# Performance work log

Hardware: AMD Instinct MI355X
Metric: run time of the kernel (lower is better)

## Reference

```python
import jax, jax.numpy as jnp
from jax import lax
import numpy as np

N_BLOCKS = 5; C = 256; K = 1024; NQ = 8; NRES = 4; B = 2; T = 65536


def conv1d(x, w, b, stride=1, padding=0, dilation=1):
    # x: [N,C,T], w: [O,I,k]
    y = lax.conv_general_dilated(x, w, (stride,), [(padding, padding)],
                                 rhs_dilation=(dilation,),
                                 dimension_numbers=('NCH', 'OIH', 'NCH'))
    return y + b[None, :, None]


def conv_transpose1d(x, w, b):
    # PyTorch ConvTranspose1d(k=4, s=2, p=1); w: [in, out, 4]
    wk = jnp.swapaxes(jnp.flip(w, -1), 0, 1)  # [out, in, 4]
    y = lax.conv_general_dilated(x, wk, (1,), [(2, 2)], lhs_dilation=(2,),
                                 dimension_numbers=('NCH', 'OIH', 'NCH'))
    return y + b[None, :, None]


def residual_model(x, w0, b0, w1, b1, dil):
    # ReLU -> dilated conv3 -> ReLU -> conv3
    h = conv1d(jax.nn.relu(x), w0, b0, padding=dil, dilation=dil)
    h = conv1d(jax.nn.relu(h), w1, b1, padding=1)
    return h


def encoder(x, d0w, d0b, dw, db, rw, rb):
    for i in range(N_BLOCKS):
        if i == 0:
            x = conv1d(x, d0w, d0b, stride=2, padding=1)
        else:
            x = conv1d(x, dw[i - 1], db[i - 1], stride=2, padding=1)
        for j in range(NRES):
            dil = 3 ** (j + 1)
            # ResidualBlock.forward: x + model(x)
            x = x + residual_model(x, rw[i, j, 0], rb[i, j, 0], rw[i, j, 1], rb[i, j, 1], dil)
    return x


def decoder(x, rw, rb, uw, ub, ulw, ulb):
    for i in range(N_BLOCKS):
        for j in range(NRES):
            dil = 3 ** (j + 1)
            # DecoderBlock: x = x + ResidualBlock(x) = x + (x + model(x))
            x = x + (x + residual_model(x, rw[i, j, 0], rb[i, j, 0], rw[i, j, 1], rb[i, j, 1], dil))
        if i == N_BLOCKS - 1:
            x = conv_transpose1d(x, ulw, ulb)
        else:
            x = conv_transpose1d(x, uw[i], ub[i])
    return x


def rvq(emb, rvq_sum, rvq_usage):
    # emb: [N, C]; eval-mode residual VQ (no EMA update)
    q = jnp.zeros_like(emb)
    commit = jnp.asarray(0.0, emb.dtype)
    codes = []
    for i in range(NQ):
        cb = rvq_sum[i] / jnp.clip(rvq_usage[i], 1e-5, None)[:, None]  # [K, C]
        res = emb - q
        # argmin of squared distance over codebook rows (||res||^2 constant per column)
        scores = jnp.sum(cb * cb, axis=1)[:, None] - 2.0 * (cb @ res.T)  # [K, N]
        c = jnp.argmin(scores, axis=0)
        eq = cb[c]  # [N, C]
        eq_st = res + lax.stop_gradient(eq - res)  # straight-through
        commit = commit + jnp.mean((lax.stop_gradient(eq_st) - res) ** 2)
        q = q + eq_st
        codes.append(c.astype(jnp.int32))
    return jnp.stack(codes, axis=1), q, commit


def setup_inputs() -> dict:
    key = jax.random.key(0)
    ks = iter(jax.random.split(key, 16))

    def W(shape, fan_in):
        return (jax.random.normal(next(ks), shape, jnp.float32) / np.float32(np.sqrt(fan_in)))

    return {
        'x': jax.random.normal(next(ks), (B, 1, T), jnp.float32),
        'enc_down0_w': W((C, 1, 4), 4),
        'enc_down0_b': jnp.zeros((C,), jnp.float32),
        'enc_down_w': W((N_BLOCKS - 1, C, C, 4), C * 4),
        'enc_down_b': jnp.zeros((N_BLOCKS - 1, C), jnp.float32),
        'enc_res_w': W((N_BLOCKS, NRES, 2, C, C, 3), C * 3),
        'enc_res_b': jnp.zeros((N_BLOCKS, NRES, 2, C), jnp.float32),
        'dec_res_w': W((N_BLOCKS, NRES, 2, C, C, 3), C * 3),
        'dec_res_b': jnp.zeros((N_BLOCKS, NRES, 2, C), jnp.float32),
        'dec_up_w': W((N_BLOCKS - 1, C, C, 4), C * 4),
        'dec_up_b': jnp.zeros((N_BLOCKS - 1, C), jnp.float32),
        'dec_up_last_w': W((C, 1, 4), C * 4),
        'dec_up_last_b': jnp.zeros((1,), jnp.float32),
        'rvq_sum': jax.random.normal(next(ks), (NQ, K, C), jnp.float32) * 0.1,
        'rvq_usage': jnp.ones((NQ, K), jnp.float32),
    }


def reference(x, enc_down0_w, enc_down0_b, enc_down_w, enc_down_b, enc_res_w, enc_res_b,
              dec_res_w, dec_res_b, dec_up_w, dec_up_b, dec_up_last_w, dec_up_last_b,
              rvq_sum, rvq_usage):
    z = encoder(x, enc_down0_w, enc_down0_b, enc_down_w, enc_down_b, enc_res_w, enc_res_b)
    Bz, Cz, Tz = z.shape
    emb = jnp.transpose(z, (0, 2, 1)).reshape(Bz * Tz, Cz)  # (b t) c
    codes, q, commit = rvq(emb, rvq_sum, rvq_usage)
    zq = jnp.transpose(q.reshape(Bz, Tz, Cz), (0, 2, 1))  # b c t
    recon = decoder(zq, dec_res_w, dec_res_b, dec_up_w, dec_up_b, dec_up_last_w, dec_up_last_b)
    return recon, codes, commit
```

## Files before the change

### kernel.cpp

```cpp
#include <hip/hip_runtime.h>
#include <cstdint>

#define DEVFN static __device__ __forceinline__
typedef unsigned short ushort_t;
typedef unsigned int uint_t;
typedef short short8 __attribute__((ext_vector_type(8)));
typedef float f32x4 __attribute__((ext_vector_type(4)));

DEVFN float bf2f(ushort_t h) { return __uint_as_float(((uint_t)h) << 16); }
DEVFN ushort_t bfhi(float f) {
    uint_t u = __float_as_uint(f);
    u += 0x7fffu + ((u >> 16) & 1u);
    return (ushort_t)(u >> 16);
}
DEVFN void fsplit(float f, ushort_t& h, ushort_t& l) {
    h = bfhi(f);
    l = bfhi(f - bf2f(h));
}
DEVFN void relu_pair(uint_t& h, uint_t& l) {
    float f0 = bf2f((ushort_t)(h & 0xffffu)) + bf2f((ushort_t)(l & 0xffffu));
    float f1 = bf2f((ushort_t)(h >> 16)) + bf2f((ushort_t)(l >> 16));
    if (f0 <= 0.f) { h &= 0xffff0000u; l &= 0xffff0000u; }
    if (f1 <= 0.f) { h &= 0x0000ffffu; l &= 0x0000ffffu; }
}

__global__ __launch_bounds__(256)
void wprep3_k(const float* __restrict__ erw, const float* __restrict__ drw,
              ushort_t* __restrict__ wH, ushort_t* __restrict__ wL)
{
    const int gid = blockIdx.x * 256 + threadIdx.x;
    const int conv = gid >> 16;
    const int rem  = gid & 65535;
    const int co = rem >> 8, ci = rem & 255;
    const float* src = (conv < 40) ? (erw + (size_t)conv * 196608)
                                   : (drw + (size_t)(conv - 40) * 196608);
    const float* p = src + ((size_t)co * 256 + ci) * 3;
    ushort_t* oh = wH + (size_t)conv * 196608 + rem;
    ushort_t* ol = wL + (size_t)conv * 196608 + rem;
#pragma unroll
    for (int k = 0; k < 3; ++k) {
        ushort_t h, l; fsplit(p[k], h, l);
        oh[k * 65536] = h; ol[k * 65536] = l;
    }
}

__global__ __launch_bounds__(256)
void wprep4_k(const float* __restrict__ edw, const float* __restrict__ duw,
              ushort_t* __restrict__ wH, ushort_t* __restrict__ wL)
{
    const int gid = blockIdx.x * 256 + threadIdx.x;
    const int conv = gid >> 16;
    const int rem  = gid & 65535;
    const int co = rem >> 8, ci = rem & 255;
    ushort_t* oh = wH + (size_t)conv * 262144 + rem;
    ushort_t* ol = wL + (size_t)conv * 262144 + rem;
#pragma unroll
    for (int k = 0; k < 4; ++k) {
        float f;
        if (conv < 4)  f = edw[(size_t)conv * 262144 + ((size_t)co * 256 + ci) * 4 + k];
        else           f = duw[(size_t)(conv - 4) * 262144 + ((size_t)ci * 256 + co) * 4 + k];
        ushort_t h, l; fsplit(f, h, l);
        oh[k * 65536] = h; ol[k * 65536] = l;
    }
}

template<int TAPS, int STRIDE, bool RELU, int NT, int DMAX, bool DBUF>
__global__ __launch_bounds__(256, (NT >= 8) ? 2 : 3)
void convs_k(const ushort_t* __restrict__ inH, const ushort_t* __restrict__ inL,
             const ushort_t* __restrict__ wH, const ushort_t* __restrict__ wL,
             const float* __restrict__ bias,
             const ushort_t* __restrict__ srcH, const ushort_t* __restrict__ srcL,
             float alpha,
             ushort_t* __restrict__ outH, ushort_t* __restrict__ outL,
             int Lin, int Lout, int dil, int pad)
{
    constexpr int ROWS = NT * 16;
    constexpr int SMAX = STRIDE * (ROWS - 1) + (TAPS - 1) * DMAX + 1;
    constexpr int XSB  = SMAX * 80;
    constexpr int NEED = DBUF ? 4 * XSB : 2 * XSB;
    constexpr int ARENA = (NEED > 16640) ? NEED : 16640;
    static_assert(!DBUF || (4 * SMAX <= TAPS * 256), "prefetch item budget");
    __shared__ __align__(16) char sarena[ARENA];

    const int tid = threadIdx.x;
    const int b = blockIdx.z;
    const int t0 = blockIdx.x * ROWS;
    const int wave = tid >> 6, lane = tid & 63;
    const int quad = lane >> 4, lr = lane & 15;
    const int cow = wave * 64;
    const size_t inbase = (size_t)b * Lin * 256;
    const int S = STRIDE * (ROWS - 1) + (TAPS - 1) * dil + 1;
    const int g0 = STRIDE * t0 - pad;

    f32x4 acc[4][NT];
#pragma unroll
    for (int m = 0; m < 4; ++m)
#pragma unroll
        for (int n = 0; n < NT; ++n) acc[m][n] = (f32x4)0.f;

    if constexpr (DBUF) {
        ushort_t (*xsH0)[40] = (ushort_t(*)[40])(sarena);
        ushort_t (*xsL0)[40] = (ushort_t(*)[40])(sarena + XSB);
        ushort_t (*xsH1)[40] = (ushort_t(*)[40])(sarena + 2 * XSB);
        ushort_t (*xsL1)[40] = (ushort_t(*)[40])(sarena + 3 * XSB);
        for (int idx = tid; idx < S * 4; idx += 256) {
            const int s = idx >> 2, p = idx & 3;
            const int t = g0 + s;
            uint4 hv = make_uint4(0, 0, 0, 0), lv = hv;
            if (t >= 0 && t < Lin) {
                const size_t g = inbase + (size_t)t * 256 + p * 8;
                hv = *(const uint4*)(inH + g);
                lv = *(const uint4*)(inL + g);
                if (RELU) {
                    relu_pair(hv.x, lv.x); relu_pair(hv.y, lv.y);
                    relu_pair(hv.z, lv.z); relu_pair(hv.w, lv.w);
                }
            }
            *(uint4*)&xsH0[s][p * 8] = hv;
            *(uint4*)&xsL0[s][p * 8] = lv;
        }
        __syncthreads();
        for (int chunk = 0; chunk < 8; ++chunk) {
            const int ci0 = chunk * 32;
            ushort_t (*xsH)[40] = (chunk & 1) ? xsH1 : xsH0;
            ushort_t (*xsL)[40] = (chunk & 1) ? xsL1 : xsL0;
            ushort_t (*xnH)[40] = (chunk & 1) ? xsH0 : xsH1;
            ushort_t (*xnL)[40] = (chunk & 1) ? xsL0 : xsL1;
            const bool pf = (chunk < 7);
#pragma unroll
            for (int tap = 0; tap < TAPS; ++tap) {
                const ushort_t* wHt = wH + (size_t)tap * 65536 + ci0 + quad * 8;
                const ushort_t* wLt = wL + (size_t)tap * 65536 + ci0 + quad * 8;
                short8 aH[4], aL[4];
#pragma unroll
                for (int m = 0; m < 4; ++m) {
                    const int co = cow + m * 16 + lr;
                    aH[m] = *(const short8*)(wHt + co * 256);
                    aL[m] = *(const short8*)(wLt + co * 256);
                }
                const int idx = tap * 256 + tid;
                const int s = idx >> 2, p = idx & 3;
                const int tr = g0 + s;
                const bool inr = (idx < S * 4);
                uint4 hv = make_uint4(0, 0, 0, 0), lv = hv;
                if (pf && inr && tr >= 0 && tr < Lin) {
                    const size_t g = inbase + (size_t)tr * 256 + (ci0 + 32) + p * 8;
                    hv = *(const uint4*)(inH + g);
                    lv = *(const uint4*)(inL + g);
                }
                const int rb = tap * dil;
#pragma unroll
                for (int n = 0; n < NT; ++n) {
                    const int srow = STRIDE * (n * 16 + lr) + rb;
                    const short8 bH = *(const short8*)&xsH[srow][quad * 8];
                    const short8 bL = *(const short8*)&xsL[srow][quad * 8];
#pragma unroll
                    for (int m = 0; m < 4; ++m)
                        acc[m][n] = __builtin_amdgcn_mfma_f32_16x16x32_bf16(aH[m], bH, acc[m][n], 0, 0, 0);
#pragma unroll
                    for (int m = 0; m < 4; ++m)
                        acc[m][n] = __builtin_amdgcn_mfma_f32_16x16x32_bf16(aH[m], bL, acc[m][n], 0, 0, 0);
#pragma unroll
                    for (int m = 0; m < 4; ++m)
                        acc[m][n] = __builtin_amdgcn_mfma_f32_16x16x32_bf16(aL[m], bH, acc[m][n], 0, 0, 0);
                }
                if (pf && inr) {
                    if (RELU) {
                        relu_pair(hv.x, lv.x); relu_pair(hv.y, lv.y);
                        relu_pair(hv.z, lv.z); relu_pair(hv.w, lv.w);
                    }
                    *(uint4*)&xnH[s][p * 8] = hv;
                    *(uint4*)&xnL[s][p * 8] = lv;
                }
            }
            __syncthreads();
        }
    } else {
        ushort_t (*xsH)[40] = (ushort_t(*)[40])(sarena);
        ushort_t (*xsL)[40] = (ushort_t(*)[40])(sarena + XSB);
        for (int chunk = 0; chunk < 8; ++chunk) {
            const int ci0 = chunk * 32;
            __syncthreads();
            for (int idx = tid; idx < S * 4; idx += 256) {
                const int s = idx >> 2, p = idx & 3;
                const int t = g0 + s;
                uint4 hv = make_uint4(0, 0, 0, 0), lv = hv;
                if (t >= 0 && t < Lin) {
                    const size_t g = inbase + (size_t)t * 256 + ci0 + p * 8;
                    hv = *(const uint4*)(inH + g);
                    lv = *(const uint4*)(inL + g);
                    if (RELU) {
                        relu_pair(hv.x, lv.x); relu_pair(hv.y, lv.y);
                        relu_pair(hv.z, lv.z); relu_pair(hv.w, lv.w);
                    }
                }
                *(uint4*)&xsH[s][p * 8] = hv;
                *(uint4*)&xsL[s][p * 8] = lv;
            }
            __syncthreads();
#pragma unroll
            for (int tap = 0; tap < TAPS; ++tap) {
                const ushort_t* wHt = wH + (size_t)tap * 65536 + ci0 + quad * 8;
                const ushort_t* wLt = wL + (size_t)tap * 65536 + ci0 + quad * 8;
                short8 aH[4], aL[4];
#pragma unroll
                for (int m = 0; m < 4; ++m) {
                    const int co = cow + m * 16 + lr;
                    aH[m] = *(const short8*)(wHt + co * 256);
                    aL[m] = *(const short8*)(wLt + co * 256);
                }
                const int rb = tap * dil;
#pragma unroll
                for (int n = 0; n < NT; ++n) {
                    const int srow = STRIDE * (n * 16 + lr) + rb;
                    const short8 bH = *(const short8*)&xsH[srow][quad * 8];
                    const short8 bL = *(const short8*)&xsL[srow][quad * 8];
#pragma unroll
                    for (int m = 0; m < 4; ++m)
                        acc[m][n] = __builtin_amdgcn_mfma_f32_16x16x32_bf16(aH[m], bH, acc[m][n], 0, 0, 0);
#pragma unroll
                    for (int m = 0; m < 4; ++m)
                        acc[m][n] = __builtin_amdgcn_mfma_f32_16x16x32_bf16(aH[m], bL, acc[m][n], 0, 0, 0);
#pragma unroll
                    for (int m = 0; m < 4; ++m)
                        acc[m][n] = __builtin_amdgcn_mfma_f32_16x16x32_bf16(aL[m], bH, acc[m][n], 0, 0, 0);
                }
            }
        }
    }
    float4 bvv[4];
#pragma unroll
    for (int m = 0; m < 4; ++m)
        bvv[m] = *(const float4*)&bias[cow + m * 16 + quad * 4];
    __syncthreads();
    float (*ebuf)[260] = (float(*)[260])sarena;
#pragma unroll
    for (int n = 0; n < NT; ++n) {
#pragma unroll
        for (int m = 0; m < 4; ++m) {
            float4 v;
            v.x = acc[m][n][0] + bvv[m].x;
            v.y = acc[m][n][1] + bvv[m].y;
            v.z = acc[m][n][2] + bvv[m].z;
            v.w = acc[m][n][3] + bvv[m].w;
            *(float4*)&ebuf[lr][cow + m * 16 + quad * 4] = v;
        }
        __syncthreads();
        {
            const int row = tid >> 4;
            const int c00 = (tid & 15) * 4;
            const int t = t0 + n * 16 + row;
            const size_t gr = ((size_t)b * Lout + t) * 256;
#pragma unroll
            for (int rep = 0; rep < 4; ++rep) {
                const int col = c00 + rep * 64;
                float4 v = *(const float4*)&ebuf[row][col];
                if (alpha != 0.f) {
                    const ushort4 sh = *(const ushort4*)(srcH + gr + col);
                    const ushort4 sl = *(const ushort4*)(srcL + gr + col);
                    v.x += alpha * (bf2f(sh.x) + bf2f(sl.x));
                    v.y += alpha * (bf2f(sh.y) + bf2f(sl.y));
                    v.z += alpha * (bf2f(sh.z) + bf2f(sl.z));
                    v.w += alpha * (bf2f(sh.w) + bf2f(sl.w));
                }
                ushort4 oh, ol;
                fsplit(v.x, oh.x, ol.x); fsplit(v.y, oh.y, ol.y);
                fsplit(v.z, oh.z, ol.z); fsplit(v.w, oh.w, ol.w);
                *(ushort4*)(outH + gr + col) = oh;
                *(ushort4*)(outL + gr + col) = ol;
            }
        }
        __syncthreads();
    }
}

template<int NTc>
__global__ __launch_bounds__(256, 2)
void convt_k(const ushort_t* __restrict__ inH, const ushort_t* __restrict__ inL,
             const ushort_t* __restrict__ wH, const ushort_t* __restrict__ wL,
             const float* __restrict__ bias,
             ushort_t* __restrict__ outH, ushort_t* __restrict__ outL, int Lin)
{
    constexpr int ROWS = NTc * 16;
    constexpr int S = ROWS + 2;
    constexpr int XSB = S * 40 * 2;
    constexpr int ARENA = (2 * XSB > 33280) ? 2 * XSB : 33280;
    __shared__ __align__(16) char sarena[ARENA];
    ushort_t (*xsH)[40] = (ushort_t(*)[40])(sarena);
    ushort_t (*xsL)[40] = (ushort_t(*)[40])(sarena + XSB);

    const int tid = threadIdx.x;
    const int b = blockIdx.z;
    const int m0 = blockIdx.x * ROWS;
    const int Lout = Lin * 2;
    const int wave = tid >> 6, lane = tid & 63;
    const int quad = lane >> 4, lr = lane & 15;
    const int cow = wave * 64;
    const size_t inbase = (size_t)b * Lin * 256;

    f32x4 acc[4][NTc][2];
#pragma unroll
    for (int m = 0; m < 4; ++m)
#pragma unroll
        for (int n = 0; n < NTc; ++n) { acc[m][n][0] = (f32x4)0.f; acc[m][n][1] = (f32x4)0.f; }

    for (int chunk = 0; chunk < 8; ++chunk) {
        const int ci0 = chunk * 32;
        __syncthreads();
        for (int idx = tid; idx < S * 4; idx += 256) {
            const int s = idx >> 2, p = idx & 3;
            const int t = m0 - 1 + s;
            uint4 hv = make_uint4(0, 0, 0, 0), lv = hv;
            if (t >= 0 && t < Lin) {
                const size_t g = inbase + (size_t)t * 256 + ci0 + p * 8;
                hv = *(const uint4*)(inH + g);
                lv = *(const uint4*)(inL + g);
            }
            *(uint4*)&xsH[s][p * 8] = hv;
            *(uint4*)&xsL[s][p * 8] = lv;
        }
        __syncthreads();
#pragma unroll
        for (int tap = 0; tap < 4; ++tap) {
            const int ph = (tap == 0 || tap == 2) ? 1 : 0;
            const int sh = (tap == 0) ? 1 : ((tap == 3) ? -1 : 0);
            const ushort_t* wHt = wH + (size_t)tap * 65536 + ci0 + quad * 8;
            const ushort_t* wLt = wL + (size_t)tap * 65536 + ci0 + quad * 8;
            short8 aH[4], aL[4];
#pragma unroll
            for (int m = 0; m < 4; ++m) {
                const int co = cow + m * 16 + lr;
                aH[m] = *(const short8*)(wHt + co * 256);
                aL[m] = *(const short8*)(wLt + co * 256);
            }
#pragma unroll
            for (int n = 0; n < NTc; ++n) {
                const int srow = n * 16 + lr + sh + 1;
                const short8 bH = *(const short8*)&xsH[srow][quad * 8];
                const short8 bL = *(const short8*)&xsL[srow][quad * 8];
#pragma unroll
                for (int m = 0; m < 4; ++m)
                    acc[m][n][ph] = __builtin_amdgcn_mfma_f32_16x16x32_bf16(aH[m], bH, acc[m][n][ph], 0, 0, 0);
#pragma unroll
                for (int m = 0; m < 4; ++m)
                    acc[m][n][ph] = __builtin_amdgcn_mfma_f32_16x16x32_bf16(aH[m], bL, acc[m][n][ph], 0, 0, 0);
#pragma unroll
                for (int m = 0; m < 4; ++m)
                    acc[m][n][ph] = __builtin_amdgcn_mfma_f32_16x16x32_bf16(aL[m], bH, acc[m][n][ph], 0, 0, 0);
            }
        }
    }
    float4 bvv[4];
#pragma unroll
    for (int m = 0; m < 4; ++m)
        bvv[m] = *(const float4*)&bias[cow + m * 16 + quad * 4];
    __syncthreads();
    float (*ebuf)[260] = (float(*)[260])sarena;
#pragma unroll
    for (int n = 0; n < NTc; ++n) {
#pragma unroll
        for (int m = 0; m < 4; ++m) {
#pragma unroll
            for (int ph = 0; ph < 2; ++ph) {
                float4 v;
                v.x = acc[m][n][ph][0] + bvv[m].x;
                v.y = acc[m][n][ph][1] + bvv[m].y;
                v.z = acc[m][n][ph][2] + bvv[m].z;
                v.w = acc[m][n][ph][3] + bvv[m].w;
                *(float4*)&ebuf[2 * lr + ph][cow + m * 16 + quad * 4] = v;
            }
        }
        __syncthreads();
        {
            const int baset = 2 * (m0 + n * 16);
#pragma unroll
            for (int h = 0; h < 8; ++h) {
                const int row = (tid >> 4) + 16 * (h >> 2);
                const int col = (tid & 15) * 4 + (h & 3) * 64;
                const int t = baset + row;
                const size_t gr = ((size_t)b * Lout + t) * 256 + col;
                float4 v = *(const float4*)&ebuf[row][col];
                ushort4 oh, ol;
                fsplit(v.x, oh.x, ol.x); fsplit(v.y, oh.y, ol.y);
                fsplit(v.z, oh.z, ol.z); fsplit(v.w, oh.w, ol.w);
                *(ushort4*)(outH + gr) = oh;
                *(ushort4*)(outL + gr) = ol;
            }
        }
        __syncthreads();
    }
}

__global__ __launch_bounds__(256)
void down0_k2(const float* __restrict__ x, const float* __restrict__ w,
              const float* __restrict__ bias,
              ushort_t* __restrict__ outH, ushort_t* __restrict__ outL)
{
    const int t = blockIdx.x;
    const int b = blockIdx.y;
    const int co = threadIdx.x;
    const float* xb = x + (size_t)b * 65536;
    const float4 wv = *(const float4*)(w + co * 4);
    float s = bias[co];
    const int ti0 = 2 * t - 1;
    if (ti0 >= 0)      s = fmaf(xb[ti0], wv.x, s);
    s = fmaf(xb[ti0 + 1], wv.y, s);
    s = fmaf(xb[ti0 + 2], wv.z, s);
    if (ti0 + 3 < 65536) s = fmaf(xb[ti0 + 3], wv.w, s);
    ushort_t h, l; fsplit(s, h, l);
    const size_t g = ((size_t)b * 32768 + t) * 256 + co;
    outH[g] = h; outL[g] = l;
}

__global__ __launch_bounds__(256)
void uplast_k2(const ushort_t* __restrict__ inH, const ushort_t* __restrict__ inL,
               const float* __restrict__ w, const float* __restrict__ bias,
               float* __restrict__ out, int Lin)
{
    const int m = blockIdx.x * 256 + threadIdx.x;
    const int b = blockIdx.y;
    const float bv = bias[0];
    float aE = bv, aO = bv;
    const size_t base = (size_t)b * Lin * 256;
    const ushort_t* r0H = inH + base + (size_t)m * 256;
    const ushort_t* r0L = inL + base + (size_t)m * 256;
    const bool hasM = (m > 0), hasP = (m + 1 < Lin);
    for (int c0 = 0; c0 < 256; c0 += 8) {
        uint4 h0 = *(const uint4*)(r0H + c0);
        uint4 l0 = *(const uint4*)(r0L + c0);
        uint4 hm = make_uint4(0,0,0,0), lm = hm, hp = hm, lp = hm;
        if (hasM) { hm = *(const uint4*)(r0H - 256 + c0); lm = *(const uint4*)(r0L - 256 + c0); }
        if (hasP) { hp = *(const uint4*)(r0H + 256 + c0); lp = *(const uint4*)(r0L + 256 + c0); }
        const uint_t* h0p = (const uint_t*)&h0; const uint_t* l0p = (const uint_t*)&l0;
        const uint_t* hmp = (const uint_t*)&hm; const uint_t* lmp = (const uint_t*)&lm;
        const uint_t* hpp = (const uint_t*)&hp; const uint_t* lpp = (const uint_t*)&lp;
#pragma unroll
        for (int e = 0; e < 4; ++e) {
#pragma unroll
            for (int half = 0; half < 2; ++half) {
                const int sh = half * 16;
                const int ci = c0 + e * 2 + half;
                const float x0  = bf2f((ushort_t)(h0p[e] >> sh)) + bf2f((ushort_t)(l0p[e] >> sh));
                const float xm1 = bf2f((ushort_t)(hmp[e] >> sh)) + bf2f((ushort_t)(lmp[e] >> sh));
                const float xp1 = bf2f((ushort_t)(hpp[e] >> sh)) + bf2f((ushort_t)(lpp[e] >> sh));
                const float4 wv = *(const float4*)(w + ci * 4);
                aE = fmaf(x0, wv.y, fmaf(xm1, wv.w, aE));
                aO = fmaf(xp1, wv.x, fmaf(x0, wv.z, aO));
            }
        }
    }
    *(float2*)(out + (size_t)b * 2 * Lin + 2 * m) = make_float2(aE, aO);
}

__global__ void emb_k(const ushort_t* __restrict__ H, const ushort_t* __restrict__ L,
                      float* __restrict__ emb)
{
    const size_t g = (size_t)blockIdx.x * 256 + threadIdx.x;
    emb[g] = bf2f(H[g]) + bf2f(L[g]);
}
__global__ void qsplit_k(const float* __restrict__ q,
                         ushort_t* __restrict__ H, ushort_t* __restrict__ L)
{
    const size_t g = (size_t)blockIdx.x * 256 + threadIdx.x;
    ushort_t h, l; fsplit(q[g], h, l);
    H[g] = h; L[g] = l;
}

__global__ __launch_bounds__(256)
void rvq_cb_k(const float* __restrict__ sum, const float* __restrict__ usage,
              float* __restrict__ cb, float* __restrict__ cbT,
              float* __restrict__ cbn, int iq)
{
    const int k = blockIdx.x, c = threadIdx.x;
    const float den = fmaxf(usage[iq * 1024 + k], 1e-5f);
    const float v = sum[((size_t)iq * 1024 + k) * 256 + c] / den;
    cb[(size_t)k * 256 + c] = v;
    cbT[(size_t)c * 1024 + k] = v;
    float s = v * v;
    for (int off = 32; off; off >>= 1) s += __shfl_down(s, off, 64);
    __shared__ float ls[4];
    if ((c & 63) == 0) ls[c >> 6] = s;
    __syncthreads();
    if (c == 0) cbn[k] = ls[0] + ls[1] + ls[2] + ls[3];
}

DEVFN unsigned int ordbits(float f)
{
    unsigned u = __float_as_uint(f);
    return (u & 0x80000000u) ? ~u : (u | 0x80000000u);
}
DEVFN unsigned long long shfl_xor_u64(unsigned long long v, int mask)
{
    int lo = (int)(v & 0xffffffffull), hi = (int)(v >> 32);
    lo = __shfl_xor(lo, mask, 64);
    hi = __shfl_xor(hi, mask, 64);
    return ((unsigned long long)(unsigned)hi << 32) | (unsigned)lo;
}

__global__ __launch_bounds__(256)
void rvq_argmin_k(const float* __restrict__ emb, const float* __restrict__ q,
                  const float* __restrict__ cbT, const float* __restrict__ cbn,
                  int* __restrict__ codes, float* __restrict__ codes_out, int iq)
{
    const int n0 = blockIdx.x * 16;
    const int tid = threadIdx.x;
    __shared__ float res[16][256];
    for (int idx = tid; idx < 16 * 256; idx += 256) {
        int nl = idx >> 8, c = idx & 255;
        size_t g = (size_t)(n0 + nl) * 256 + c;
        res[nl][c] = emb[g] - q[g];
    }
    __syncthreads();
    float dot[16][4];
#pragma unroll
    for (int nl = 0; nl < 16; ++nl)
#pragma unroll
        for (int j = 0; j < 4; ++j) dot[nl][j] = 0.f;

    const float* cbtp = cbT + tid * 4;
    for (int c = 0; c < 256; ++c) {
        const float4 cbv = *(const float4*)(cbtp + (size_t)c * 1024);
#pragma unroll
        for (int nl = 0; nl < 16; ++nl) {
            const float r = res[nl][c];
            dot[nl][0] = fmaf(cbv.x, r, dot[nl][0]);
            dot[nl][1] = fmaf(cbv.y, r, dot[nl][1]);
            dot[nl][2] = fmaf(cbv.z, r, dot[nl][2]);
            dot[nl][3] = fmaf(cbv.w, r, dot[nl][3]);
        }
    }
    const float4 nrm = *(const float4*)(cbn + tid * 4);
    __shared__ unsigned long long wred[4][16];
    const int wave = tid >> 6, lane = tid & 63;
#pragma unroll
    for (int nl = 0; nl < 16; ++nl) {
        float s0 = nrm.x - 2.f * dot[nl][0];
        float s1 = nrm.y - 2.f * dot[nl][1];
        float s2 = nrm.z - 2.f * dot[nl][2];
        float s3 = nrm.w - 2.f * dot[nl][3];
        unsigned long long key =
            ((unsigned long long)ordbits(s0) << 32) | (unsigned)(tid * 4 + 0);
        unsigned long long k1 =
            ((unsigned long long)ordbits(s1) << 32) | (unsigned)(tid * 4 + 1);
        unsigned long long k2 =
            ((unsigned long long)ordbits(s2) << 32) | (unsigned)(tid * 4 + 2);
        unsigned long long k3 =
            ((unsigned long long)ordbits(s3) << 32) | (unsigned)(tid * 4 + 3);
        if (k1 < key) key = k1;
        if (k2 < key) key = k2;
        if (k3 < key) key = k3;
        for (int off = 32; off; off >>= 1) {
            unsigned long long o = shfl_xor_u64(key, off);
            if (o < key) key = o;
        }
        if (lane == 0) wred[wave][nl] = key;
    }
    __syncthreads();
    if (tid < 16) {
        unsigned long long bkey = wred[0][tid];
        if (wred[1][tid] < bkey) bkey = wred[1][tid];
        if (wred[2][tid] < bkey) bkey = wred[2][tid];
        if (wred[3][tid] < bkey) bkey = wred[3][tid];
        const int code = (int)(bkey & 0xffffffffull);
        codes[(size_t)(n0 + tid) * 8 + iq] = code;
        codes_out[(size_t)(n0 + tid) * 8 + iq] = (float)code;
    }
}

__global__ __launch_bounds__(256)
void rvq_update_k(const float* __restrict__ emb, float* __restrict__ q,
                  const float* __restrict__ cb, const int* __restrict__ codes,
                  float* __restrict__ commit, int iq)
{
    const int n = blockIdx.x, c = threadIdx.x;
    const int code = codes[(size_t)n * 8 + iq];
    const size_t g = (size_t)n * 256 + c;
    const float qv = q[g] + cb[(size_t)code * 256 + c];
    q[g] = qv;
    const float e = qv - emb[g];
    float s = e * e;
    for (int off = 32; off; off >>= 1) s += __shfl_down(s, off, 64);
    __shared__ float ls[4];
    if ((c & 63) == 0) ls[c >> 6] = s;
    __syncthreads();
    if (c == 0) atomicAdd(commit, ls[0] + ls[1] + ls[2] + ls[3]);
}

__global__ void commit_write_k(const float* __restrict__ commit, float* __restrict__ out)
{
    out[0] = commit[0] * (1.f / (4096.f * 256.f));
}

extern "C" void kernel_launch(void* const* d_in, const int* in_sizes, int n_in,
                              void* d_out, int out_size, void* d_ws, size_t ws_size,
                              hipStream_t stream)
{
    const float* x    = (const float*)d_in[0];
    const float* ed0w = (const float*)d_in[1];
    const float* ed0b = (const float*)d_in[2];
    const float* edw  = (const float*)d_in[3];
    const float* edb  = (const float*)d_in[4];
    const float* erw  = (const float*)d_in[5];
    const float* erb  = (const float*)d_in[6];
    const float* drw  = (const float*)d_in[7];
    const float* drb  = (const float*)d_in[8];
    const float* duw  = (const float*)d_in[9];
    const float* dub  = (const float*)d_in[10];
    const float* dulw = (const float*)d_in[11];
    const float* dulb = (const float*)d_in[12];
    const float* rsum = (const float*)d_in[13];
    const float* rusg = (const float*)d_in[14];
    float* out = (float*)d_out;

    char* base = (char*)d_ws;
    size_t o = 0;
    ushort_t* wH3 = (ushort_t*)(base + o); o += 31457280;
    ushort_t* wL3 = (ushort_t*)(base + o); o += 31457280;
    ushort_t* w4H = (ushort_t*)(base + o); o += 4194304;
    ushort_t* w4L = (ushort_t*)(base + o); o += 4194304;
    ushort_t* AH  = (ushort_t*)(base + o); o += 33554432;
    ushort_t* AL  = (ushort_t*)(base + o); o += 33554432;
    ushort_t* BH  = (ushort_t*)(base + o); o += 33554432;
    ushort_t* BL  = (ushort_t*)(base + o); o += 33554432;
    float* emb    = (float*)(base + o);    o += 4194304;
    float* q      = (float*)(base + o);    o += 4194304;
    float* commit = (float*)(base + o);    o += 64;
    float* cb     = (float*)(base + o);    o += 1048576;
    float* cbT    = (float*)(base + o);    o += 1048576;
    float* cbn    = (float*)(base + o);    o += 4096;
    int*   codes  = (int*)(base + o);      o += 131072;

    static const int DIL[4] = {3, 9, 27, 81};

    hipMemsetAsync(q, 0, 4194304 + 64, stream);

    wprep3_k<<<20480, 256, 0, stream>>>(erw, drw, wH3, wL3);
    wprep4_k<<<2048, 256, 0, stream>>>(edw, duw, w4H, w4L);

    auto conv3 = [&](const ushort_t* iH, const ushort_t* iL,
                     const ushort_t* wh, const ushort_t* wl, const float* bb,
                     const ushort_t* sH, const ushort_t* sL, float alpha,
                     ushort_t* oH, ushort_t* oL, int L, int d) {
        const bool db = (d <= 27);
        if (L >= 16384) {
            if (db) convs_k<3, 1, true, 8, 27, true><<<dim3(L / 128, 1, 2), 256, 0, stream>>>(
                        iH, iL, wh, wl, bb, sH, sL, alpha, oH, oL, L, L, d, d);
            else    convs_k<3, 1, true, 8, 81, false><<<dim3(L / 128, 1, 2), 256, 0, stream>>>(
                        iH, iL, wh, wl, bb, sH, sL, alpha, oH, oL, L, L, d, d);
        } else if (L >= 8192) {
            if (db) convs_k<3, 1, true, 4, 27, true><<<dim3(L / 64, 1, 2), 256, 0, stream>>>(
                        iH, iL, wh, wl, bb, sH, sL, alpha, oH, oL, L, L, d, d);
            else    convs_k<3, 1, true, 4, 81, false><<<dim3(L / 64, 1, 2), 256, 0, stream>>>(
                        iH, iL, wh, wl, bb, sH, sL, alpha, oH, oL, L, L, d, d);
        } else if (L >= 4096) {
            if (db) convs_k<3, 1, true, 2, 27, true><<<dim3(L / 32, 1, 2), 256, 0, stream>>>(
                        iH, iL, wh, wl, bb, sH, sL, alpha, oH, oL, L, L, d, d);
            else    convs_k<3, 1, true, 2, 81, false><<<dim3(L / 32, 1, 2), 256, 0, stream>>>(
                        iH, iL, wh, wl, bb, sH, sL, alpha, oH, oL, L, L, d, d);
        } else {
            if (db) convs_k<3, 1, true, 1, 27, true><<<dim3(L / 16, 1, 2), 256, 0, stream>>>(
                        iH, iL, wh, wl, bb, sH, sL, alpha, oH, oL, L, L, d, d);
            else    convs_k<3, 1, true, 1, 81, false><<<dim3(L / 16, 1, 2), 256, 0, stream>>>(
                        iH, iL, wh, wl, bb, sH, sL, alpha, oH, oL, L, L, d, d);
        }
    };

    down0_k2<<<dim3(32768, 2), 256, 0, stream>>>(x, ed0w, ed0b, AH, AL);
    int L = 32768;
    for (int i = 0; i < 5; ++i) {
        if (i > 0) {
            const ushort_t* wh = w4H + (size_t)(i - 1) * 262144;
            const ushort_t* wl = w4L + (size_t)(i - 1) * 262144;
            const int Lout = L / 2;
            if (Lout >= 16384)
                convs_k<4, 2, false, 8, 1, false><<<dim3(Lout / 128, 1, 2), 256, 0, stream>>>(
                    AH, AL, wh, wl, edb + (i - 1) * 256, AH, AL, 0.f, BH, BL, L, Lout, 1, 1);
            else if (Lout >= 8192)
                convs_k<4, 2, false, 4, 1, false><<<dim3(Lout / 64, 1, 2), 256, 0, stream>>>(
                    AH, AL, wh, wl, edb + (i - 1) * 256, AH, AL, 0.f, BH, BL, L, Lout, 1, 1);
            else if (Lout >= 4096)
                convs_k<4, 2, false, 2, 1, false><<<dim3(Lout / 32, 1, 2), 256, 0, stream>>>(
                    AH, AL, wh, wl, edb + (i - 1) * 256, AH, AL, 0.f, BH, BL, L, Lout, 1, 1);
            else
                convs_k<4, 2, false, 1, 1, false><<<dim3(Lout / 16, 1, 2), 256, 0, stream>>>(
                    AH, AL, wh, wl, edb + (i - 1) * 256, AH, AL, 0.f, BH, BL, L, Lout, 1, 1);
            ushort_t* t;
            t = AH; AH = BH; BH = t;
            t = AL; AL = BL; BL = t;
            L = Lout;
        }
        for (int j = 0; j < 4; ++j) {
            const int d = DIL[j];
            const size_t u = (size_t)(i * 4 + j) * 2;
            conv3(AH, AL, wH3 + (u + 0) * 196608, wL3 + (u + 0) * 196608,
                  erb + (u + 0) * 256, AH, AL, 0.f, BH, BL, L, d);
            conv3(BH, BL, wH3 + (u + 1) * 196608, wL3 + (u + 1) * 196608,
                  erb + (u + 1) * 256, AH, AL, 1.f, AH, AL, L, 1);
        }
    }

    emb_k<<<4096, 256, 0, stream>>>(AH, AL, emb);
    for (int iq = 0; iq < 8; ++iq) {
        rvq_cb_k<<<1024, 256, 0, stream>>>(rsum, rusg, cb, cbT, cbn, iq);
        rvq_argmin_k<<<256, 256, 0, stream>>>(emb, q, cbT, cbn, codes, out + 131072, iq);
        rvq_update_k<<<4096, 256, 0, stream>>>(emb, q, cb, codes, commit, iq);
    }
    qsplit_k<<<4096, 256, 0, stream>>>(q, AH, AL);

    L = 2048;
    for (int i = 0; i < 5; ++i) {
        for (int j = 0; j < 4; ++j) {
            const int d = DIL[j];
            const size_t u = 40 + (size_t)(i * 4 + j) * 2;
            conv3(AH, AL, wH3 + (u + 0) * 196608, wL3 + (u + 0) * 196608,
                  drb + ((size_t)(i * 4 + j) * 2 + 0) * 256, AH, AL, 0.f, BH, BL, L, d);
            conv3(BH, BL, wH3 + (u + 1) * 196608, wL3 + (u + 1) * 196608,
                  drb + ((size_t)(i * 4 + j) * 2 + 1) * 256, AH, AL, 2.f, AH, AL, L, 1);
        }
        if (i < 4) {
            const ushort_t* wh = w4H + (size_t)(4 + i) * 262144;
            const ushort_t* wl = w4L + (size_t)(4 + i) * 262144;
            if (L >= 8192)
                convt_k<4><<<dim3(L / 64, 1, 2), 256, 0, stream>>>(
                    AH, AL, wh, wl, dub + i * 256, BH, BL, L);
            else if (L >= 4096)
                convt_k<2><<<dim3(L / 32, 1, 2), 256, 0, stream>>>(
                    AH, AL, wh, wl, dub + i * 256, BH, BL, L);
            else
                convt_k<1><<<dim3(L / 16, 1, 2), 256, 0, stream>>>(
                    AH, AL, wh, wl, dub + i * 256, BH, BL, L);
            ushort_t* t;
            t = AH; AH = BH; BH = t;
            t = AL; AL = BL; BL = t;
            L *= 2;
        } else {
            uplast_k2<<<dim3(L / 256, 2), 256, 0, stream>>>(AH, AL, dulw, dulb, out, L);
        }
    }

    commit_write_k<<<1, 1, 0, stream>>>(commit, out + 163840);
}
```

Measured before the change: 6.007 ms.

## Fuse RVQ argmin with quantizer update and swizzle conv block order across XCDs

The RVQ update step (accumulate the chosen codebook row into q and add to the commitment loss) now runs at the end of the argmin kernel, reusing the residual already in shared memory. This removes one launch per quantizer stage and the re-read of emb and q. The conv and transposed-conv kernels also remap blockIdx.x so that consecutive time tiles land on the same XCD, which is meant to improve L2 reuse of overlapping halos. The commit loss is now computed as (cb - r)^2 rather than (q_new - emb)^2, which can round slightly differently.

```diff
diff --git a/kernel.cpp b/kernel.cpp
--- a/kernel.cpp
+++ b/kernel.cpp
@@ -22,6 +22,9 @@
     float f1 = bf2f((ushort_t)(h >> 16)) + bf2f((ushort_t)(l >> 16));
     if (f0 <= 0.f) { h &= 0xffff0000u; l &= 0xffff0000u; }
     if (f1 <= 0.f) { h &= 0x0000ffffu; l &= 0x0000ffffu; }
+}
+DEVFN int xcd_swz(int bx, int gx) {
+    return ((gx & 7) == 0) ? ((bx & 7) * (gx >> 3) + (bx >> 3)) : bx;
 }
 
 __global__ __launch_bounds__(256)
@@ -84,7 +87,7 @@
 
     const int tid = threadIdx.x;
     const int b = blockIdx.z;
-    const int t0 = blockIdx.x * ROWS;
+    const int t0 = xcd_swz(blockIdx.x, gridDim.x) * ROWS;
     const int wave = tid >> 6, lane = tid & 63;
     const int quad = lane >> 4, lr = lane & 15;
     const int cow = wave * 64;
@@ -291,7 +294,7 @@
 
     const int tid = threadIdx.x;
     const int b = blockIdx.z;
-    const int m0 = blockIdx.x * ROWS;
+    const int m0 = xcd_swz(blockIdx.x, gridDim.x) * ROWS;
     const int Lout = Lin * 2;
     const int wave = tid >> 6, lane = tid & 63;
     const int quad = lane >> 4, lr = lane & 15;
@@ -498,9 +501,11 @@
 }
 
 __global__ __launch_bounds__(256)
-void rvq_argmin_k(const float* __restrict__ emb, const float* __restrict__ q,
-                  const float* __restrict__ cbT, const float* __restrict__ cbn,
-                  int* __restrict__ codes, float* __restrict__ codes_out, int iq)
+void rvq_argmin_upd_k(const float* __restrict__ emb, float* __restrict__ q,
+                      const float* __restrict__ cb, const float* __restrict__ cbT,
+                      const float* __restrict__ cbn,
+                      int* __restrict__ codes, float* __restrict__ codes_out,
+                      float* __restrict__ commit, int iq)
 {
     const int n0 = blockIdx.x * 16;
     const int tid = threadIdx.x;
@@ -531,6 +536,7 @@
     }
     const float4 nrm = *(const float4*)(cbn + tid * 4);
     __shared__ unsigned long long wred[4][16];
+    __shared__ int scode[16];
     const int wave = tid >> 6, lane = tid & 63;
 #pragma unroll
     for (int nl = 0; nl < 16; ++nl) {
@@ -562,28 +568,27 @@
         if (wred[2][tid] < bkey) bkey = wred[2][tid];
         if (wred[3][tid] < bkey) bkey = wred[3][tid];
         const int code = (int)(bkey & 0xffffffffull);
+        scode[tid] = code;
         codes[(size_t)(n0 + tid) * 8 + iq] = code;
         codes_out[(size_t)(n0 + tid) * 8 + iq] = (float)code;
     }
-}
-
-__global__ __launch_bounds__(256)
-void rvq_update_k(const float* __restrict__ emb, float* __restrict__ q,
-                  const float* __restrict__ cb, const int* __restrict__ codes,
-                  float* __restrict__ commit, int iq)
-{
-    const int n = blockIdx.x, c = threadIdx.x;
-    const int code = codes[(size_t)n * 8 + iq];
-    const size_t g = (size_t)n * 256 + c;
-    const float qv = q[g] + cb[(size_t)code * 256 + c];
-    q[g] = qv;
-    const float e = qv - emb[g];
-    float s = e * e;
-    for (int off = 32; off; off >>= 1) s += __shfl_down(s, off, 64);
-    __shared__ float ls[4];
-    if ((c & 63) == 0) ls[c >> 6] = s;
     __syncthreads();
-    if (c == 0) atomicAdd(commit, ls[0] + ls[1] + ls[2] + ls[3]);
+    float csum = 0.f;
+#pragma unroll 4
+    for (int nl = 0; nl < 16; ++nl) {
+        const int code = scode[nl];
+        const float cbv = cb[(size_t)code * 256 + tid];
+        const float r = res[nl][tid];
+        const size_t g = (size_t)(n0 + nl) * 256 + tid;
+        q[g] = emb[g] - r + cbv;
+        const float e = cbv - r;
+        csum = fmaf(e, e, csum);
+    }
+    for (int off = 32; off; off >>= 1) csum += __shfl_down(csum, off, 64);
+    __shared__ float ls2[4];
+    if ((tid & 63) == 0) ls2[tid >> 6] = csum;
+    __syncthreads();
+    if (tid == 0) atomicAdd(commit, ls2[0] + ls2[1] + ls2[2] + ls2[3]);
 }
 
 __global__ void commit_write_k(const float* __restrict__ commit, float* __restrict__ out)
@@ -702,8 +707,8 @@
     emb_k<<<4096, 256, 0, stream>>>(AH, AL, emb);
     for (int iq = 0; iq < 8; ++iq) {
         rvq_cb_k<<<1024, 256, 0, stream>>>(rsum, rusg, cb, cbT, cbn, iq);
-        rvq_argmin_k<<<256, 256, 0, stream>>>(emb, q, cbT, cbn, codes, out + 131072, iq);
-        rvq_update_k<<<4096, 256, 0, stream>>>(emb, q, cb, codes, commit, iq);
+        rvq_argmin_upd_k<<<256, 256, 0, stream>>>(emb, q, cb, cbT, cbn,
+                                                  codes, out + 131072, commit, iq);
     }
     qsplit_k<<<4096, 256, 0, stream>>>(q, AH, AL);
 
```

Measured after the change: 5.454 ms. 1.1x faster.
